# Kernel tuning notes

Hardware: AMD Instinct MI355X
Metric: run time of the kernel (lower is better)

Reference implementation:

```python
import jax, jax.numpy as jnp
import numpy as np

N = 50000          # nodes
E = 1_600_000      # edges (avg degree 32)
F_IN = 128         # num_node_features
HID = 128          # hidden_dim
G = 512            # graphs in batch
NEG_SLOPE = 0.2    # PyG GATConv default


def setup_inputs() -> dict:
    key = jax.random.key(0)
    ks = jax.random.split(key, 13)
    s_in = 1.0 / np.sqrt(F_IN)
    s_h = 1.0 / np.sqrt(HID)
    return {
        "x": jax.random.normal(ks[0], (N, F_IN), jnp.float32),
        "edge_index": jax.random.randint(ks[1], (2, E), 0, N, dtype=jnp.int32),
        "batch": jnp.sort(jax.random.randint(ks[2], (N,), 0, G, dtype=jnp.int32)),
        "W1": jax.random.normal(ks[3], (F_IN, HID), jnp.float32) * s_in,
        "a_src1": jax.random.normal(ks[4], (HID,), jnp.float32) * s_h,
        "a_dst1": jax.random.normal(ks[5], (HID,), jnp.float32) * s_h,
        "b1": jnp.zeros((HID,), jnp.float32),
        "W2": jax.random.normal(ks[6], (HID, HID), jnp.float32) * s_h,
        "a_src2": jax.random.normal(ks[7], (HID,), jnp.float32) * s_h,
        "a_dst2": jax.random.normal(ks[8], (HID,), jnp.float32) * s_h,
        "b2": jnp.zeros((HID,), jnp.float32),
        "fc_w": jax.random.normal(ks[9], (2 * HID, 1), jnp.float32) * (1.0 / np.sqrt(2 * HID)),
        "fc_b": jnp.zeros((1,), jnp.float32),
    }


def _gat_conv(x, W, a_src, a_dst, b, src, dst, n):
    # PyG GATConv, heads=1: h = xW; alpha_e = softmax_dst(leaky_relu(a_s.h[src] + a_d.h[dst]))
    h = x @ W                                    # [N, C]
    asrc = h @ a_src                             # [N]
    adst = h @ a_dst                             # [N]
    logits = jax.nn.leaky_relu(asrc[src] + adst[dst], NEG_SLOPE)  # [E']
    m = jax.ops.segment_max(logits, dst, num_segments=n)
    ex = jnp.exp(logits - m[dst])
    denom = jax.ops.segment_sum(ex, dst, num_segments=n)
    alpha = ex / denom[dst]                      # segment softmax over incoming edges
    out = jax.ops.segment_sum(h[src] * alpha[:, None], dst, num_segments=n)
    return out + b


def reference(x, edge_index, batch, W1, a_src1, a_dst1, b1, W2, a_src2, a_dst2, b2, fc_w, fc_b):
    n = x.shape[0]
    loop = jnp.arange(n, dtype=edge_index.dtype)   # add_self_loops=True (PyG default)
    src = jnp.concatenate([edge_index[0], loop])
    dst = jnp.concatenate([edge_index[1], loop])

    h = jax.nn.relu(x)
    h = jax.nn.relu(_gat_conv(h, W1, a_src1, a_dst1, b1, src, dst, n))
    h = jax.nn.relu(_gat_conv(h, W2, a_src2, a_dst2, b2, src, dst, n))

    counts = jax.ops.segment_sum(jnp.ones((n,), h.dtype), batch, num_segments=G)
    maxp = jax.ops.segment_max(h, batch, num_segments=G)
    maxp = jnp.where(counts[:, None] > 0, maxp, 0.0)
    meanp = jax.ops.segment_sum(h, batch, num_segments=G) / jnp.maximum(counts, 1.0)[:, None]
    pooled = jnp.concatenate([maxp, meanp], axis=1)  # [G, 2*HID]
    return pooled @ fc_w + fc_b                      # [G, 1]
```

## Files before the change

### kernel.cpp

```cpp
#include <hip/hip_runtime.h>
#include <math.h>


#define LEAKY 0.2f
#define CAP 128
#define CAPB 20480

typedef short bf16x8 __attribute__((ext_vector_type(8)));
typedef float f32x4 __attribute__((ext_vector_type(4)));

__device__ __forceinline__ unsigned short f2bf(float x) {
    unsigned int u = __float_as_uint(x);
    unsigned int r = (u + 0x7FFFu + ((u >> 16) & 1u)) >> 16;
    return (unsigned short)r;
}
__device__ __forceinline__ float bf2f(unsigned short b) {
    return __uint_as_float((unsigned int)b << 16);
}

__global__ __launch_bounds__(256, 5) void gemmscat(
        const float* __restrict__ A,
        const float* __restrict__ W,
        unsigned short* __restrict__ Cb,
        const float* __restrict__ a_src,
        const float* __restrict__ a_dst,
        float* __restrict__ asv,
        float* __restrict__ adv,
        int n, int applyRelu, int gemmBlocks,
        const int* __restrict__ ei,
        int* __restrict__ binCnt,
        unsigned* __restrict__ binBuf,
        int E) {
    __shared__ __align__(16) unsigned short Bt[2][64 * 128];

    if ((int)blockIdx.x >= gemmBlocks) {
        int* lcnt  = (int*)Bt;
        int* gbase = ((int*)Bt) + 128;
        const int bb = (int)blockIdx.x - gemmBlocks;
        const int base = bb * 4096;
        const int tid = threadIdx.x;
        const int nbins = (n + 511) >> 9;
        if (tid < nbins) lcnt[tid] = 0;
        __syncthreads();

        int4 dv[4], sv[4];
        int ok[4];
#pragma unroll
        for (int t = 0; t < 4; ++t) {
            int i0 = base + t * 1024 + tid * 4;
            ok[t] = (i0 < E);
            if (ok[t]) {
                dv[t] = *(const int4*)(ei + (size_t)E + i0);
                sv[t] = *(const int4*)(ei + i0);
            }
        }
        int rr[16];
        unsigned pk[16];
#pragma unroll
        for (int t = 0; t < 4; ++t) {
            int dd[4] = { dv[t].x, dv[t].y, dv[t].z, dv[t].w };
            int ss[4] = { sv[t].x, sv[t].y, sv[t].z, sv[t].w };
#pragma unroll
            for (int q = 0; q < 4; ++q) {
                int j = t * 4 + q;
                rr[j] = -1;
                if (ok[t]) {
                    unsigned d = (unsigned)dd[q];
                    pk[j] = (d << 16) | (unsigned)ss[q];
                    rr[j] = atomicAdd(&lcnt[d >> 9], 1);
                }
            }
        }
        __syncthreads();
        if (tid < nbins)
            gbase[tid] = (lcnt[tid] > 0) ? atomicAdd(&binCnt[tid], lcnt[tid]) : 0;
        __syncthreads();
#pragma unroll
        for (int j = 0; j < 16; ++j) {
            if (rr[j] >= 0) {
                int b = (int)(pk[j] >> 25);
                int pos = gbase[b] + rr[j];
                if (pos < CAPB) binBuf[(size_t)b * CAPB + pos] = pk[j];
            }
        }
        return;
    }

    const int tid = threadIdx.x;
    const int wv = tid >> 6;
    const int lane = tid & 63;
    const int cl = lane & 15;
    const int kg = lane >> 4;

    const int row0 = blockIdx.x * 64;
    const int row = row0 + wv * 16 + cl;
    bf16x8 ahi[4], alo[4];
#pragma unroll
    for (int ks = 0; ks < 4; ++ks) {
        int k0 = ks * 32 + kg * 8;
        float vv[8] = {0.f, 0.f, 0.f, 0.f, 0.f, 0.f, 0.f, 0.f};
        if (row < n) {
            float4 v0 = *(const float4*)(A + (size_t)row * 128 + k0);
            float4 v1 = *(const float4*)(A + (size_t)row * 128 + k0 + 4);
            vv[0] = v0.x; vv[1] = v0.y; vv[2] = v0.z; vv[3] = v0.w;
            vv[4] = v1.x; vv[5] = v1.y; vv[6] = v1.z; vv[7] = v1.w;
            if (applyRelu) {
#pragma unroll
                for (int u = 0; u < 8; ++u) vv[u] = fmaxf(vv[u], 0.f);
            }
        }
#pragma unroll
        for (int u = 0; u < 8; ++u) {
            unsigned short h = f2bf(vv[u]);
            ahi[ks][u] = (short)h;
            alo[ks][u] = (short)f2bf(vv[u] - bf2f(h));
        }
    }

    f32x4 acc[8];
#pragma unroll
    for (int ci = 0; ci < 8; ++ci) {
        acc[ci][0] = 0.f; acc[ci][1] = 0.f; acc[ci][2] = 0.f; acc[ci][3] = 0.f;
    }

#pragma unroll
    for (int h = 0; h < 2; ++h) {
        __syncthreads();
        {
            int c64 = tid & 63;
            int c = h * 64 + c64;
            int kh = tid >> 6;
#pragma unroll
            for (int j = 0; j < 4; ++j) {
                int kb = kh * 32 + j * 8;
                unsigned short thi[8], tlo[8];
#pragma unroll
                for (int u = 0; u < 8; ++u) {
                    float v = W[(size_t)(kb + u) * 128 + c];
                    unsigned short hh = f2bf(v);
                    thi[u] = hh;
                    tlo[u] = f2bf(v - bf2f(hh));
                }
                int byteoff = (c64 * 256 + kb * 2) ^ ((c64 & 7) << 4);
                *(uint4*)((char*)Bt[0] + byteoff) = *(const uint4*)thi;
                *(uint4*)((char*)Bt[1] + byteoff) = *(const uint4*)tlo;
            }
        }
        __syncthreads();
#pragma unroll
        for (int ks = 0; ks < 4; ++ks) {
            int k0 = ks * 32 + kg * 8;
#pragma unroll
            for (int ct = 0; ct < 4; ++ct) {
                int c64 = ct * 16 + cl;
                int byteoff = (c64 * 256 + k0 * 2) ^ ((c64 & 7) << 4);
                bf16x8 bhi = *(const bf16x8*)((const char*)Bt[0] + byteoff);
                bf16x8 blo = *(const bf16x8*)((const char*)Bt[1] + byteoff);
                int ci = h * 4 + ct;
                acc[ci] = __builtin_amdgcn_mfma_f32_16x16x32_bf16(
                    ahi[ks], bhi, acc[ci], 0, 0, 0);
                acc[ci] = __builtin_amdgcn_mfma_f32_16x16x32_bf16(
                    ahi[ks], blo, acc[ci], 0, 0, 0);
                acc[ci] = __builtin_amdgcn_mfma_f32_16x16x32_bf16(
                    alo[ks], bhi, acc[ci], 0, 0, 0);
            }
        }
    }

    {
        float ps[4] = {0.f, 0.f, 0.f, 0.f};
        float pd[4] = {0.f, 0.f, 0.f, 0.f};
#pragma unroll
        for (int ci = 0; ci < 8; ++ci) {
            float as_ = a_src[ci * 16 + cl];
            float ad_ = a_dst[ci * 16 + cl];
#pragma unroll
            for (int r = 0; r < 4; ++r) {
                ps[r] += acc[ci][r] * as_;
                pd[r] += acc[ci][r] * ad_;
            }
        }
#pragma unroll
        for (int r = 0; r < 4; ++r) {
#pragma unroll
            for (int off = 1; off < 16; off <<= 1) {
                ps[r] += __shfl_xor(ps[r], off, 64);
                pd[r] += __shfl_xor(pd[r], off, 64);
            }
        }
        if (cl == 0) {
#pragma unroll
            for (int r = 0; r < 4; ++r) {
                int rr = row0 + wv * 16 + kg * 4 + r;
                if (rr < n) { asv[rr] = ps[r]; adv[rr] = pd[r]; }
            }
        }
    }

    __syncthreads();
    unsigned short* Cst = Bt[0];
#pragma unroll
    for (int ci = 0; ci < 8; ++ci) {
#pragma unroll
        for (int r = 0; r < 4; ++r)
            Cst[(wv * 16 + kg * 4 + r) * 128 + ci * 16 + cl] = f2bf(acc[ci][r]);
    }
    __syncthreads();
    {
        int r = tid >> 2, cb = (tid & 3) * 32;
        int grow = row0 + r;
        if (grow < n) {
            uint4* dst = (uint4*)(Cb + (size_t)grow * 128 + cb);
            const uint4* src = (const uint4*)(Cst + r * 128 + cb);
            dst[0] = src[0]; dst[1] = src[1]; dst[2] = src[2]; dst[3] = src[3];
        }
    }
}

__global__ __launch_bounds__(512) void binbuild(const unsigned* __restrict__ binBuf,
                                                const int* __restrict__ binCnt,
                                                unsigned short* __restrict__ col,
                                                int* __restrict__ cnt, int n) {
    __shared__ int lc[512];
    const int b = blockIdx.x;
    const int lo = b << 9;
    const int tid = threadIdx.x;
    lc[tid] = 0;
    __syncthreads();
    int m = binCnt[b];
    if (m > CAPB) m = CAPB;
    for (int i = tid; i < m; i += 512) {
        unsigned u = binBuf[(size_t)b * CAPB + i];
        int d = (int)(u >> 16);
        int s = (int)(u & 0xFFFFu);
        int p = atomicAdd(&lc[d - lo], 1);
        if (p < CAP) col[(size_t)d * CAP + p] = (unsigned short)s;
    }
    __syncthreads();
    int d = lo + tid;
    if (d < n) cnt[d] = lc[tid];
}

__global__ __launch_bounds__(256) void aggregate(const unsigned short* __restrict__ hb,
                                                 const int* __restrict__ cnt,
                                                 const unsigned short* __restrict__ col,
                                                 const float* __restrict__ asv,
                                                 const float* __restrict__ adv,
                                                 const float* __restrict__ bias,
                                                 float* __restrict__ out, int n) {
    __shared__ uint2 spk[4][128];
    const int wv = threadIdx.x >> 6;
    const int lane = threadIdx.x & 63;
    const int w = blockIdx.x * 4 + wv;
    if (w >= n) return;
    int deg = cnt[w];
    if (deg > CAP - 1) deg = CAP - 1;
    const int D = deg + 1;
    const size_t start = (size_t)w * CAP;
    const float ad = adv[w];

    int c0 = (lane < deg) ? (int)col[start + lane] : w;
    int c1 = (64 + lane < deg) ? (int)col[start + 64 + lane] : w;
    float l0 = -INFINITY, l1 = -INFINITY;
    if (lane < D) {
        l0 = asv[c0] + ad;
        l0 = l0 > 0.f ? l0 : LEAKY * l0;
    }
    if (64 + lane < D) {
        l1 = asv[c1] + ad;
        l1 = l1 > 0.f ? l1 : LEAKY * l1;
    }
    float m = fmaxf(l0, l1);
#pragma unroll
    for (int off = 32; off; off >>= 1) m = fmaxf(m, __shfl_xor(m, off, 64));
    float e0 = (lane < D) ? __expf(l0 - m) : 0.f;
    float e1 = (64 + lane < D) ? __expf(l1 - m) : 0.f;
    float s = e0 + e1;
#pragma unroll
    for (int off = 32; off; off >>= 1) s += __shfl_xor(s, off, 64);
    float inv = 1.f / s;
    spk[wv][lane]      = make_uint2((unsigned)c0, __float_as_uint(e0));
    spk[wv][64 + lane] = make_uint2((unsigned)c1, __float_as_uint(e1));

    const int hw = lane >> 5;
    const int sl = lane & 31;
    const ushort4* hb4 = (const ushort4*)hb;
    float4 aa[8];
#pragma unroll
    for (int j = 0; j < 8; ++j) aa[j] = make_float4(0.f, 0.f, 0.f, 0.f);
    for (int i = 0; i < D; i += 16) {
        int cs[8]; float ws[8];
#pragma unroll
        for (int j = 0; j < 8; ++j) {
            uint2 p = spk[wv][i + 2 * j + hw];
            cs[j] = (int)p.x;
            ws[j] = __uint_as_float(p.y);
        }
        ushort4 rs[8];
#pragma unroll
        for (int j = 0; j < 8; ++j)
            rs[j] = hb4[cs[j] * 32 + sl];
#pragma unroll
        for (int j = 0; j < 8; ++j) {
            aa[j].x += ws[j] * bf2f(rs[j].x);
            aa[j].y += ws[j] * bf2f(rs[j].y);
            aa[j].z += ws[j] * bf2f(rs[j].z);
            aa[j].w += ws[j] * bf2f(rs[j].w);
        }
    }
#pragma unroll
    for (int j = 1; j < 8; ++j) {
        aa[0].x += aa[j].x; aa[0].y += aa[j].y;
        aa[0].z += aa[j].z; aa[0].w += aa[j].w;
    }
    aa[0].x += __shfl_xor(aa[0].x, 32);
    aa[0].y += __shfl_xor(aa[0].y, 32);
    aa[0].z += __shfl_xor(aa[0].z, 32);
    aa[0].w += __shfl_xor(aa[0].w, 32);
    if (hw == 0) {
        float4 b = ((const float4*)bias)[sl];
        float4 o;
        o.x = fmaxf(aa[0].x * inv + b.x, 0.f);
        o.y = fmaxf(aa[0].y * inv + b.y, 0.f);
        o.z = fmaxf(aa[0].z * inv + b.z, 0.f);
        o.w = fmaxf(aa[0].w * inv + b.w, 0.f);
        *((float4*)(out + (size_t)w * 128) + sl) = o;
    }
}

__global__ __launch_bounds__(128) void poolfc(const float* __restrict__ h2,
                                              const int* __restrict__ batch,
                                              const float* __restrict__ fcw,
                                              const float* __restrict__ fcb,
                                              float* __restrict__ out, int G, int n) {
    __shared__ int seg[2];
    int g = blockIdx.x;
    int f = threadIdx.x;
    if (f < 2) {
        int target = g + f;
        int lo = 0, hi = n;
        while (lo < hi) {
            int mid = (lo + hi) >> 1;
            if (batch[mid] < target) lo = mid + 1; else hi = mid;
        }
        seg[f] = lo;
    }
    __syncthreads();
    int s = seg[0], e = seg[1];
    float m = -INFINITY, sum = 0.f;
    for (int node = s; node < e; ++node) {
        float v = h2[(size_t)node * 128 + f];
        m = fmaxf(m, v);
        sum += v;
    }
    int cnt = e - s;
    float maxp = (cnt > 0) ? m : 0.f;
    float cden = (float)(cnt > 0 ? cnt : 1);
    float meanp = sum / cden;
    float p = maxp * fcw[f] + meanp * fcw[128 + f];
    __shared__ float red[128];
    red[f] = p;
    __syncthreads();
    for (int off = 64; off; off >>= 1) {
        if (f < off) red[f] += red[f + off];
        __syncthreads();
    }
    if (f == 0) out[g] = red[0] + fcb[0];
}

extern "C" void kernel_launch(void* const* d_in, const int* in_sizes, int n_in,
                              void* d_out, int out_size, void* d_ws, size_t ws_size,
                              hipStream_t stream) {
    const int N = in_sizes[0] / 128;
    const int E = in_sizes[1] / 2;
    const int G = out_size;

    const float* x      = (const float*)d_in[0];
    const int*   ei     = (const int*)d_in[1];
    const int*   batch  = (const int*)d_in[2];
    const float* W1     = (const float*)d_in[3];
    const float* a_src1 = (const float*)d_in[4];
    const float* a_dst1 = (const float*)d_in[5];
    const float* b1     = (const float*)d_in[6];
    const float* W2     = (const float*)d_in[7];
    const float* a_src2 = (const float*)d_in[8];
    const float* a_dst2 = (const float*)d_in[9];
    const float* b2     = (const float*)d_in[10];
    const float* fcw    = (const float*)d_in[11];
    const float* fcb    = (const float*)d_in[12];
    float* out = (float*)d_out;

    const int NBINS = (N + 511) >> 9;

    char* wp = (char*)d_ws;
    auto alloc = [&](size_t bytes) -> void* {
        void* p = (void*)wp;
        wp += (bytes + 255) & ~(size_t)255;
        return p;
    };
    int* cnt        = (int*)alloc(sizeof(int) * N);
    int* binCnt     = (int*)alloc(sizeof(int) * 128);
    unsigned* binBuf = (unsigned*)alloc(sizeof(unsigned) * (size_t)NBINS * CAPB);
    unsigned short* col = (unsigned short*)alloc(sizeof(unsigned short) * (size_t)N * CAP);
    float* ha    = (float*)alloc(sizeof(float) * (size_t)N * 128);
    unsigned short* hb = (unsigned short*)alloc(sizeof(unsigned short) * (size_t)N * 128);
    float* asv   = (float*)alloc(sizeof(float) * N);
    float* adv   = (float*)alloc(sizeof(float) * N);

    hipMemsetAsync(binCnt, 0, sizeof(int) * 128, stream);

    const int gemmGrid = (N + 63) / 64;
    const int waveGrid = (N + 3) / 4;
    const int binGrid  = (E + 4095) / 4096;

    gemmscat<<<gemmGrid + binGrid, 256, 0, stream>>>(
        x, W1, hb, a_src1, a_dst1, asv, adv, N, 1, gemmGrid, ei,
        binCnt, binBuf, E);
    binbuild<<<NBINS, 512, 0, stream>>>(binBuf, binCnt, col, cnt, N);
    aggregate<<<waveGrid, 256, 0, stream>>>(hb, cnt, col, asv, adv, b1, ha, N);

    gemmscat<<<gemmGrid, 256, 0, stream>>>(
        ha, W2, hb, a_src2, a_dst2, asv, adv, N, 0, gemmGrid, ei,
        binCnt, binBuf, E);
    aggregate<<<waveGrid, 256, 0, stream>>>(hb, cnt, col, asv, adv, b2, ha, N);

    poolfc<<<G, 128, 0, stream>>>(ha, batch, fcw, fcb, out, G, N);
}
```

Measured before the change: 324.0 us.

## Split GAT aggregation across four blocks per node by feature slice

Each aggregate block now handles a 32-feature slice of four nodes, so the grid is four times larger. Within a wave, lanes are arranged as 8 edge rows by 8 feature columns and partial sums are reduced with shuffles. Column-index loads and output stores use nontemporal hints. The aim is more parallel waves to hide the latency of gathering neighbour features. The cost is that the softmax logits, max and sum are recomputed four times per node, and each gathered row fetch shrinks to 64-byte pieces.

```diff
diff --git a/kernel.cpp b/kernel.cpp
--- a/kernel.cpp
+++ b/kernel.cpp
@@ -251,7 +251,8 @@
     __shared__ uint2 spk[4][128];
     const int wv = threadIdx.x >> 6;
     const int lane = threadIdx.x & 63;
-    const int w = blockIdx.x * 4 + wv;
+    const int s = blockIdx.x & 3;
+    const int w = (blockIdx.x >> 2) * 4 + wv;
     if (w >= n) return;
     int deg = cnt[w];
     if (deg > CAP - 1) deg = CAP - 1;
@@ -259,8 +260,8 @@
     const size_t start = (size_t)w * CAP;
     const float ad = adv[w];
 
-    int c0 = (lane < deg) ? (int)col[start + lane] : w;
-    int c1 = (64 + lane < deg) ? (int)col[start + 64 + lane] : w;
+    int c0 = (lane < deg) ? (int)__builtin_nontemporal_load(col + start + lane) : w;
+    int c1 = (64 + lane < deg) ? (int)__builtin_nontemporal_load(col + start + 64 + lane) : w;
     float l0 = -INFINITY, l1 = -INFINITY;
     if (lane < D) {
         l0 = asv[c0] + ad;
@@ -275,56 +276,45 @@
     for (int off = 32; off; off >>= 1) m = fmaxf(m, __shfl_xor(m, off, 64));
     float e0 = (lane < D) ? __expf(l0 - m) : 0.f;
     float e1 = (64 + lane < D) ? __expf(l1 - m) : 0.f;
-    float s = e0 + e1;
-#pragma unroll
-    for (int off = 32; off; off >>= 1) s += __shfl_xor(s, off, 64);
-    float inv = 1.f / s;
+    float sm = e0 + e1;
+#pragma unroll
+    for (int off = 32; off; off >>= 1) sm += __shfl_xor(sm, off, 64);
+    float inv = 1.f / sm;
     spk[wv][lane]      = make_uint2((unsigned)c0, __float_as_uint(e0));
     spk[wv][64 + lane] = make_uint2((unsigned)c1, __float_as_uint(e1));
 
-    const int hw = lane >> 5;
-    const int sl = lane & 31;
+    const int rg = lane >> 3;
+    const int oc = lane & 7;
     const ushort4* hb4 = (const ushort4*)hb;
-    float4 aa[8];
-#pragma unroll
-    for (int j = 0; j < 8; ++j) aa[j] = make_float4(0.f, 0.f, 0.f, 0.f);
-    for (int i = 0; i < D; i += 16) {
-        int cs[8]; float ws[8];
+    const int sbase = s * 8 + oc;
+    float a0 = 0.f, a1 = 0.f, a2 = 0.f, a3 = 0.f;
+    for (int i = 0; i < D; i += 64) {
 #pragma unroll
         for (int j = 0; j < 8; ++j) {
-            uint2 p = spk[wv][i + 2 * j + hw];
-            cs[j] = (int)p.x;
-            ws[j] = __uint_as_float(p.y);
-        }
-        ushort4 rs[8];
-#pragma unroll
-        for (int j = 0; j < 8; ++j)
-            rs[j] = hb4[cs[j] * 32 + sl];
-#pragma unroll
-        for (int j = 0; j < 8; ++j) {
-            aa[j].x += ws[j] * bf2f(rs[j].x);
-            aa[j].y += ws[j] * bf2f(rs[j].y);
-            aa[j].z += ws[j] * bf2f(rs[j].z);
-            aa[j].w += ws[j] * bf2f(rs[j].w);
-        }
-    }
-#pragma unroll
-    for (int j = 1; j < 8; ++j) {
-        aa[0].x += aa[j].x; aa[0].y += aa[j].y;
-        aa[0].z += aa[j].z; aa[0].w += aa[j].w;
-    }
-    aa[0].x += __shfl_xor(aa[0].x, 32);
-    aa[0].y += __shfl_xor(aa[0].y, 32);
-    aa[0].z += __shfl_xor(aa[0].z, 32);
-    aa[0].w += __shfl_xor(aa[0].w, 32);
-    if (hw == 0) {
-        float4 b = ((const float4*)bias)[sl];
-        float4 o;
-        o.x = fmaxf(aa[0].x * inv + b.x, 0.f);
-        o.y = fmaxf(aa[0].y * inv + b.y, 0.f);
-        o.z = fmaxf(aa[0].z * inv + b.z, 0.f);
-        o.w = fmaxf(aa[0].w * inv + b.w, 0.f);
-        *((float4*)(out + (size_t)w * 128) + sl) = o;
+            uint2 p = spk[wv][(i + j * 8 + rg) & 127];
+            ushort4 r = hb4[(int)p.x * 32 + sbase];
+            float wt = __uint_as_float(p.y);
+            a0 += wt * bf2f(r.x);
+            a1 += wt * bf2f(r.y);
+            a2 += wt * bf2f(r.z);
+            a3 += wt * bf2f(r.w);
+        }
+    }
+#pragma unroll
+    for (int off = 8; off < 64; off <<= 1) {
+        a0 += __shfl_xor(a0, off, 64);
+        a1 += __shfl_xor(a1, off, 64);
+        a2 += __shfl_xor(a2, off, 64);
+        a3 += __shfl_xor(a3, off, 64);
+    }
+    if (rg == 0) {
+        float4 b = *((const float4*)(bias + s * 32) + oc);
+        f32x4 o;
+        o[0] = fmaxf(a0 * inv + b.x, 0.f);
+        o[1] = fmaxf(a1 * inv + b.y, 0.f);
+        o[2] = fmaxf(a2 * inv + b.z, 0.f);
+        o[3] = fmaxf(a3 * inv + b.w, 0.f);
+        __builtin_nontemporal_store(o, (f32x4*)(out + (size_t)w * 128 + s * 32) + oc);
     }
 }
 
@@ -411,18 +401,19 @@
 
     const int gemmGrid = (N + 63) / 64;
     const int waveGrid = (N + 3) / 4;
+    const int aggGrid  = waveGrid * 4;
     const int binGrid  = (E + 4095) / 4096;
 
     gemmscat<<<gemmGrid + binGrid, 256, 0, stream>>>(
         x, W1, hb, a_src1, a_dst1, asv, adv, N, 1, gemmGrid, ei,
         binCnt, binBuf, E);
     binbuild<<<NBINS, 512, 0, stream>>>(binBuf, binCnt, col, cnt, N);
-    aggregate<<<waveGrid, 256, 0, stream>>>(hb, cnt, col, asv, adv, b1, ha, N);
+    aggregate<<<aggGrid, 256, 0, stream>>>(hb, cnt, col, asv, adv, b1, ha, N);
 
     gemmscat<<<gemmGrid, 256, 0, stream>>>(
         ha, W2, hb, a_src2, a_dst2, asv, adv, N, 0, gemmGrid, ei,
         binCnt, binBuf, E);
-    aggregate<<<waveGrid, 256, 0, stream>>>(hb, cnt, col, asv, adv, b2, ha, N);
+    aggregate<<<aggGrid, 256, 0, stream>>>(hb, cnt, col, asv, adv, b2, ha, N);
 
     poolfc<<<G, 128, 0, stream>>>(ha, batch, fcw, fcb, out, G, N);
 }
```

Result: slower. 446.8 us (+37.9%).
